# Kernel optimization log

Measured on AMD Instinct MI355X. Metric: run time of the kernel, lower is better.

The kernel has to match this reference:

```python
import jax, jax.numpy as jnp
import numpy as np
import math

H = 5120        # hidden_size
NH = 32         # num heads
HD = H // NH    # head_dim = 160
B = 1
S = 2048
TRAIN_SEQLEN = 8192
BASE = 10000.0


def _rotary_cos_sin(seq_len):
    # Eval-mode RotaryEmbedding: seq_len clamped to training_seqlen, NTK alpha + mscale (logN) scaling.
    eff = max(seq_len, TRAIN_SEQLEN)
    scale = eff / TRAIN_SEQLEN
    mscale = 1.0 if scale <= 1.0 else 0.1 * math.log(scale) + 1.0
    ntk_alpha = max(2 ** math.ceil(math.log(eff / 4096, 2) + 1) - 1, 1)
    base = BASE * ntk_alpha ** (HD / (HD - 2))
    inv_freq = 1.0 / base ** (np.arange(0, HD, 2, dtype=np.float64) / HD)
    t = np.arange(eff, dtype=np.float64)
    freqs = np.outer(t, inv_freq)              # [eff, HD/2]
    emb = np.concatenate([freqs, freqs], axis=-1)  # [eff, HD]
    cos = (mscale * np.cos(emb))[:seq_len].astype(np.float32)
    sin = (mscale * np.sin(emb))[:seq_len].astype(np.float32)
    return jnp.asarray(cos), jnp.asarray(sin)


def _rotate_half(x):
    x1, x2 = x[..., : HD // 2], x[..., HD // 2 :]
    return jnp.concatenate([-x2, x1], axis=-1)


def setup_inputs() -> dict:
    key = jax.random.key(0)
    ks = jax.random.split(key, 6)
    hidden_states = jax.random.normal(ks[0], (B, S, H), jnp.float32)
    residual = jax.random.normal(ks[1], (B, S, H), jnp.float32)
    # boolean causal mask, True = masked (matches masked_fill semantics)
    attention_mask = jnp.triu(jnp.ones((S, S), dtype=bool), k=1)[None, None]
    Wq = jax.random.normal(ks[2], (H, H), jnp.float32) * 0.02      # query: Linear(h, h, bias=False)
    Wkv = jax.random.normal(ks[3], (2 * H, H), jnp.float32) * 0.02  # key_value: Linear(h, 2h, bias=False)
    Wd = jax.random.normal(ks[4], (H, H), jnp.float32) * 0.02       # dense: Linear(h, h) with bias
    bd = jnp.zeros((H,), jnp.float32)
    return {
        "hidden_states": hidden_states,
        "residual": residual,
        "attention_mask": attention_mask,
        "Wq": Wq,
        "Wkv": Wkv,
        "Wd": Wd,
        "bd": bd,
    }


def reference(hidden_states, residual, attention_mask, Wq, Wkv, Wd, bd):
    b, s, h = hidden_states.shape
    # QKV projections (torch Linear: y = x @ W.T)
    q = jnp.einsum('bsh,oh->bso', hidden_states, Wq).reshape(b, s, NH, HD)
    kv = jnp.einsum('bsh,oh->bso', hidden_states, Wkv).reshape(b, s, NH, 2 * HD)
    k, v = kv[..., :HD], kv[..., HD:]
    # rotary embedding with logN mscale folded into cos/sin
    cos, sin = _rotary_cos_sin(s)               # [s, HD]
    cos = cos[None, :, None, :]
    sin = sin[None, :, None, :]
    q = q * cos + _rotate_half(q) * sin
    k = k * cos + _rotate_half(k) * sin
    inv_norm = 1.0 / math.sqrt(HD)
    scores = jnp.einsum('bqnd,bknd->bnqk', q, k) * inv_norm   # [b, nh, s, s]
    scores = jnp.where(attention_mask, jnp.finfo(scores.dtype).min, scores)
    probs = jax.nn.softmax(scores, axis=-1)
    # attention_dropout p=0.0 -> identity
    ctx = jnp.einsum('bnqk,bknd->bqnd', probs, v).reshape(b, s, h)
    out = ctx @ Wd.T + bd
    # dropout_add with hidden_dropout=0.0 (eval) -> residual + out
    return residual + out
```

## Files before the change

### kernel.cpp

```cpp
#include <hip/hip_runtime.h>
#include <cmath>

typedef unsigned short u16;
typedef unsigned int   u32;

using bf16x8 = __attribute__((ext_vector_type(8))) short;
using f32x4  = __attribute__((ext_vector_type(4))) float;

#define S_LEN 2048
#define NHEAD 32
#define HDIM  160
#define HID   5120
#define NQKV  15360

__device__ __forceinline__ f32x4 mfma16(bf16x8 a, bf16x8 b, f32x4 c) {
  return __builtin_amdgcn_mfma_f32_16x16x32_bf16(a, b, c, 0, 0, 0);
}

__device__ __forceinline__ u16 f2bf(float f) {
  u32 u = __builtin_bit_cast(u32, f);
  u += 0x7FFFu + ((u >> 16) & 1u);
  return (u16)(u >> 16);
}
__device__ __forceinline__ float bf2f(u16 h) {
  u32 u = ((u32)h) << 16;
  return __builtin_bit_cast(float, u);
}

__device__ __forceinline__ void gload16(const void* g, void* l) {
  __builtin_amdgcn_global_load_lds((const __attribute__((address_space(1))) void*)g,
                                   (__attribute__((address_space(3))) void*)l, 16, 0, 0);
}

__global__ void cvt_all_kernel(const float* __restrict__ hs, const float* __restrict__ Wq,
                               const float* __restrict__ Wkv, const float* __restrict__ Wd,
                               u16* __restrict__ Xb, u16* __restrict__ Wqkvb,
                               u16* __restrict__ Wdb) {
  const int n_hs = S_LEN * HID / 8;
  const int n_q  = HID * HID / 8;
  const int n_kv = 2 * HID * HID / 8;
  const int n_d  = HID * HID / 8;
  const int total = n_hs + n_q + n_kv + n_d;
  for (int i = blockIdx.x * 256 + threadIdx.x; i < total; i += gridDim.x * 256) {
    const float* src; u16* dst; int j = i;
    if (j < n_hs)                { src = hs;  dst = Xb; }
    else if ((j -= n_hs) < n_q)  { src = Wq;  dst = Wqkvb; }
    else if ((j -= n_q) < n_kv)  { src = Wkv; dst = Wqkvb + (size_t)HID * HID; }
    else { j -= n_kv;              src = Wd;  dst = Wdb; }
    float4 a = ((const float4*)src)[(size_t)j * 2];
    float4 b = ((const float4*)src)[(size_t)j * 2 + 1];
    uint4 o;
    o.x = (u32)f2bf(a.x) | ((u32)f2bf(a.y) << 16);
    o.y = (u32)f2bf(a.z) | ((u32)f2bf(a.w) << 16);
    o.z = (u32)f2bf(b.x) | ((u32)f2bf(b.y) << 16);
    o.w = (u32)f2bf(b.z) | ((u32)f2bf(b.w) << 16);
    ((uint4*)dst)[j] = o;
  }
}

__global__ void rope_table_kernel(float2* __restrict__ tab) {
  __shared__ double invf_s[80];
  int tid = threadIdx.x;
  if (tid < 80) {
    double base = 10000.0 * pow(3.0, 160.0 / 158.0);
    invf_s[tid] = pow(base, -((double)(2 * tid)) / 160.0);
  }
  __syncthreads();
  for (int i = blockIdx.x * 256 + tid; i < S_LEN * 80; i += gridDim.x * 256) {
    int s = i / 80, j = i % 80;
    double ang = fmod((double)s * invf_s[j], 6.283185307179586476925287);
    float a = (float)ang;
    tab[i] = make_float2(cosf(a), sinf(a));
  }
}

__global__ void rope_apply2_kernel(const u16* __restrict__ qkv, const float2* __restrict__ tab,
                                   u16* __restrict__ Qr, u16* __restrict__ Kr) {
  const int n = S_LEN * NHEAD * 80;
  int i = blockIdx.x * 256 + threadIdx.x;
  bool isK = i >= n;
  if (isK) i -= n;
  const u16* src = qkv + (isK ? HID : 0);
  int headStride = isK ? 2 * HDIM : HDIM;
  u16* dst = isK ? Kr : Qr;

  int dp = i % 80; int sh = i / 80; int h = sh % NHEAD; int s = sh / NHEAD;
  int d = 2 * dp;
  const u16* row = src + (size_t)s * NQKV + h * headStride;
  u32 q01 = *(const u32*)&row[d];
  u32 p01 = *(const u32*)&row[d < 80 ? d + 80 : d - 80];
  int j = (d < 80) ? d : d - 80;
  float2 cs0 = tab[s * 80 + j];
  float2 cs1 = tab[s * 80 + j + 1];
  float q0 = bf2f((u16)(q01 & 0xffff)), q1 = bf2f((u16)(q01 >> 16));
  float p0 = bf2f((u16)(p01 & 0xffff)), p1 = bf2f((u16)(p01 >> 16));
  float sgn = (d < 80) ? -1.f : 1.f;
  float o0 = q0 * cs0.x + sgn * p0 * cs0.y;
  float o1 = q1 * cs1.x + sgn * p1 * cs1.y;
  u32 o = (u32)f2bf(o0) | ((u32)f2bf(o1) << 16);
  *(u32*)&dst[((size_t)h * S_LEN + s) * HDIM + d] = o;
}

__global__ void vtrans_kernel(const u16* __restrict__ src, u16* __restrict__ Vt, int rowStride) {
  __shared__ u16 T[HDIM][72];
  int h = blockIdx.y; int s0 = blockIdx.x * 64; int tid = threadIdx.x;
  for (int i = tid; i < 64 * 80; i += 256) {
    int s = i / 80, dp = i % 80;
    u32 v = *(const u32*)&src[(size_t)(s0 + s) * rowStride + h * 320 + 2 * dp];
    T[2 * dp][s]     = (u16)(v & 0xffff);
    T[2 * dp + 1][s] = (u16)(v >> 16);
  }
  __syncthreads();
  for (int i = tid; i < HDIM * 32; i += 256) {
    int d = i / 32, sp = i % 32;
    u32 v = (u32)T[d][2 * sp] | ((u32)T[d][2 * sp + 1] << 16);
    *(u32*)&Vt[((size_t)h * HDIM + d) * S_LEN + s0 + 2 * sp] = v;
  }
}

template<int EPI>
__global__ __launch_bounds__(512, 4) void gemm256(
    const u16* __restrict__ A, const u16* __restrict__ Bm, void* __restrict__ Cout,
    int M, int N, int K, const float* __restrict__ bias, const float* __restrict__ resid)
{
  __shared__ u16 As[2][8192];
  __shared__ u16 Bs[2][4096];
  int tid = threadIdx.x;
  int w = tid >> 6, l = tid & 63, l15 = l & 15, l4 = l >> 4;
  int wr = w >> 1, wc = w & 1;

  int nbx = gridDim.x;
  int nwg = nbx * gridDim.y;
  int lin = blockIdx.y * nbx + blockIdx.x;
  int cpx = nwg >> 3;
  int swz = (lin & 7) * cpx + (lin >> 3);
  int bm = (swz / nbx) * 256, bn = (swz % nbx) * 128;

  int srow = tid >> 2;
  int scol = ((tid & 3) * 8) ^ ((srow & 8) ? 16 : 0);
  const u16* gA0 = A + (size_t)(bm + srow) * K + scol;
  const u16* gA1 = gA0 + (size_t)128 * K;
  const u16* gB  = Bm + (size_t)(bn + srow) * K + scol;
  int w512 = w * 512;

  f32x4 acc[4][4];
#pragma unroll
  for (int i = 0; i < 4; i++)
#pragma unroll
    for (int j = 0; j < 4; j++) acc[i][j] = f32x4{0.f, 0.f, 0.f, 0.f};

  int cA = (l4 * 8) ^ ((l15 & 8) ? 16 : 0);
  const int NT = K >> 5;
  int arow = wr * 64;
  int brow = wc * 64;

  auto STAGE = [&](int kt) { int p = kt & 1, ko = kt << 5;
    gload16(gA0 + ko, &As[p][w512]);
    gload16(gA1 + ko, &As[p][4096 + w512]);
    gload16(gB  + ko, &Bs[p][w512]);
  };

  STAGE(0);
  for (int kt = 0; kt < NT; ++kt) {
    int p = kt & 1;
    if (kt + 1 < NT) {
      STAGE(kt + 1);
      asm volatile("s_waitcnt vmcnt(3)" ::: "memory");
    } else {
      asm volatile("s_waitcnt vmcnt(0)" ::: "memory");
    }
    __builtin_amdgcn_s_barrier();

    bf16x8 aF[4], bF[4];
#pragma unroll
    for (int mi = 0; mi < 4; ++mi)
      aF[mi] = *(const bf16x8*)&As[p][(arow + mi * 16 + l15) * 32 + cA];
#pragma unroll
    for (int ni = 0; ni < 4; ++ni)
      bF[ni] = *(const bf16x8*)&Bs[p][(brow + ni * 16 + l15) * 32 + cA];
    __builtin_amdgcn_s_setprio(1);
#pragma unroll
    for (int mi = 0; mi < 4; ++mi)
#pragma unroll
      for (int ni = 0; ni < 4; ++ni)
        acc[mi][ni] = mfma16(aF[mi], bF[ni], acc[mi][ni]);
    __builtin_amdgcn_s_setprio(0);
    __builtin_amdgcn_s_barrier();
  }

#pragma unroll
  for (int mi = 0; mi < 4; ++mi)
#pragma unroll
    for (int ni = 0; ni < 4; ++ni) {
      int row0 = bm + wr * 64 + mi * 16 + l4 * 4;
      int col  = bn + wc * 64 + ni * 16 + l15;
      if (EPI == 0) {
        u16* C = (u16*)Cout;
#pragma unroll
        for (int r = 0; r < 4; r++) C[(size_t)(row0 + r) * N + col] = f2bf(acc[mi][ni][r]);
      } else {
        float* C = (float*)Cout;
        float b = bias[col];
#pragma unroll
        for (int r = 0; r < 4; r++) {
          size_t idx = (size_t)(row0 + r) * N + col;
          C[idx] = acc[mi][ni][r] + b + resid[idx];
        }
      }
    }
}

template<int EPI>
__global__ __launch_bounds__(256, 2) void gemm_bt(
    const u16* __restrict__ A, const u16* __restrict__ Bm, void* __restrict__ Cout,
    int M, int N, int K, const float* __restrict__ bias, const float* __restrict__ resid)
{
  int tid = threadIdx.x;
  int wv = tid >> 6, l = tid & 63, l15 = l & 15, l4 = l >> 4;
  int nbx = gridDim.x;
  int nwg = nbx * gridDim.y;
  int lin = blockIdx.y * nbx + blockIdx.x;
  int cpx = nwg >> 3;
  int swz = (lin & 7) * cpx + (lin >> 3);
  int bm = (swz / nbx) * 128, bn = (swz % nbx) * 128;

  __shared__ u16 As[128 * 32], Bs[128 * 32];
  f32x4 acc[4][4];
#pragma unroll
  for (int i = 0; i < 4; i++)
#pragma unroll
    for (int j = 0; j < 4; j++) acc[i][j] = f32x4{0.f, 0.f, 0.f, 0.f};

  int wm = (wv >> 1) * 64, wn = (wv & 1) * 64;
  const u16* gA = A + (size_t)(bm + (tid >> 2)) * K + (tid & 3) * 8;
  const u16* gB = Bm + (size_t)(bn + (tid >> 2)) * K + (tid & 3) * 8;
  u16* ldsA = As + wv * 16 * 32;
  u16* ldsB = Bs + wv * 16 * 32;

  for (int k0 = 0; k0 < K; k0 += 32) {
    __syncthreads();
    gload16(gA + k0, ldsA);
    gload16(gA + (size_t)64 * K + k0, ldsA + 64 * 32);
    gload16(gB + k0, ldsB);
    gload16(gB + (size_t)64 * K + k0, ldsB + 64 * 32);
    __syncthreads();
    bf16x8 af[4], bfr[4];
#pragma unroll
    for (int i = 0; i < 4; i++) af[i] = *(const bf16x8*)&As[(wm + i * 16 + l15) * 32 + l4 * 8];
#pragma unroll
    for (int i = 0; i < 4; i++) bfr[i] = *(const bf16x8*)&Bs[(wn + i * 16 + l15) * 32 + l4 * 8];
#pragma unroll
    for (int mi = 0; mi < 4; mi++)
#pragma unroll
      for (int ni = 0; ni < 4; ni++) acc[mi][ni] = mfma16(af[mi], bfr[ni], acc[mi][ni]);
  }

#pragma unroll
  for (int mi = 0; mi < 4; mi++)
#pragma unroll
    for (int ni = 0; ni < 4; ni++) {
      int row0 = bm + wm + mi * 16 + l4 * 4;
      int col  = bn + wn + ni * 16 + l15;
      if (EPI == 0) {
        u16* C = (u16*)Cout;
#pragma unroll
        for (int r = 0; r < 4; r++) C[(size_t)(row0 + r) * N + col] = f2bf(acc[mi][ni][r]);
      } else {
        float* C = (float*)Cout;
        float b = bias[col];
#pragma unroll
        for (int r = 0; r < 4; r++) {
          size_t idx = (size_t)(row0 + r) * N + col;
          C[idx] = acc[mi][ni][r] + b + resid[idx];
        }
      }
    }
}

__global__ __launch_bounds__(256, 2) void attn_kernel(
    const u16* __restrict__ Qr, const u16* __restrict__ Kr,
    const u16* __restrict__ Vt, u16* __restrict__ ctx)
{
  int lin = blockIdx.x;
  int h  = lin & 31;
  int qx = (lin < 256) ? (15 - (lin >> 5)) : ((lin - 256) >> 5);
  int q0 = qx * 128;
  int tid = threadIdx.x;
  int w = tid >> 6, l = tid & 63, l15 = l & 15, l4 = l >> 4;
  int qb = q0 + w * 32;

  __shared__ u16 Ks[64][164];
  __shared__ u16 Plds[4][32][68];

  const u16* Qh = Qr + (size_t)h * S_LEN * HDIM;
  const u16* Kh = Kr + (size_t)h * S_LEN * HDIM;
  const u16* Vh = Vt + (size_t)h * HDIM * S_LEN;

  bf16x8 aQ[2][5];
#pragma unroll
  for (int mi = 0; mi < 2; mi++)
#pragma unroll
    for (int kc = 0; kc < 5; kc++)
      aQ[mi][kc] = *(const bf16x8*)&Qh[(size_t)(qb + mi * 16 + l15) * HDIM + kc * 32 + l4 * 8];

  f32x4 accO[2][10];
#pragma unroll
  for (int mi = 0; mi < 2; mi++)
#pragma unroll
    for (int dt = 0; dt < 10; dt++) accO[mi][dt] = f32x4{0.f, 0.f, 0.f, 0.f};
  float mrun[2][4], lrun[2][4];
#pragma unroll
  for (int mi = 0; mi < 2; mi++)
#pragma unroll
    for (int r = 0; r < 4; r++) { mrun[mi][r] = -1e30f; lrun[mi][r] = 0.f; }

  const float c2 = 0.07905694150420949f * 1.44269504088896f;
  int Tend = 2 * qx + 2;

  {
    uint4 rg[5];
#pragma unroll
    for (int i = 0; i < 5; i++) {
      int u = tid + 256 * i;
      int row = u / 20, c = u % 20;
      rg[i] = *(const uint4*)&Kh[(size_t)row * HDIM + c * 8];
    }
#pragma unroll
    for (int i = 0; i < 5; i++) {
      int u = tid + 256 * i;
      int row = u / 20, c = u % 20;
      *(uint4*)&Ks[row][c * 8] = rg[i];
    }
  }
  __syncthreads();

  for (int t = 0; t < Tend; ++t) {
    int k0 = t * 64;
    bool more = (t + 1 < Tend);
    uint4 rg[5];
    if (more) {
      int k1 = k0 + 64;
#pragma unroll
      for (int i = 0; i < 5; i++) {
        int u = tid + 256 * i;
        int row = u / 20, c = u % 20;
        rg[i] = *(const uint4*)&Kh[(size_t)(k1 + row) * HDIM + c * 8];
      }
    }

    if (k0 <= qb + 31) {
      f32x4 s_[2][4];
#pragma unroll
      for (int mi = 0; mi < 2; mi++)
#pragma unroll
        for (int nt = 0; nt < 4; nt++) s_[mi][nt] = f32x4{0.f, 0.f, 0.f, 0.f};

#pragma unroll
      for (int kc = 0; kc < 5; kc++) {
        bf16x8 bK[4];
#pragma unroll
        for (int nt = 0; nt < 4; nt++)
          bK[nt] = *(const bf16x8*)&Ks[nt * 16 + l15][kc * 32 + l4 * 8];
        __builtin_amdgcn_s_setprio(1);
#pragma unroll
        for (int mi = 0; mi < 2; mi++)
#pragma unroll
          for (int nt = 0; nt < 4; nt++)
            s_[mi][nt] = mfma16(aQ[mi][kc], bK[nt], s_[mi][nt]);
        __builtin_amdgcn_s_setprio(0);
      }

      if (k0 + 63 > qb) {
#pragma unroll
        for (int mi = 0; mi < 2; mi++)
#pragma unroll
          for (int nt = 0; nt < 4; nt++)
#pragma unroll
            for (int r = 0; r < 4; r++) {
              int kk = k0 + nt * 16 + l15;
              int qq = qb + mi * 16 + l4 * 4 + r;
              if (kk > qq) s_[mi][nt][r] = -1e30f;
            }
      }

#pragma unroll
      for (int mi = 0; mi < 2; mi++) {
        float sf[4];
#pragma unroll
        for (int r = 0; r < 4; r++) {
          float v = fmaxf(fmaxf(s_[mi][0][r], s_[mi][1][r]), fmaxf(s_[mi][2][r], s_[mi][3][r]));
#pragma unroll
          for (int m = 1; m <= 8; m <<= 1) v = fmaxf(v, __shfl_xor(v, m));
          float mnew = fmaxf(mrun[mi][r], v);
          sf[r] = exp2f((mrun[mi][r] - mnew) * c2);
          mrun[mi][r] = mnew;
        }
        float rsum[4] = {0.f, 0.f, 0.f, 0.f};
#pragma unroll
        for (int nt = 0; nt < 4; nt++)
#pragma unroll
          for (int r = 0; r < 4; r++) {
            float p = exp2f((s_[mi][nt][r] - mrun[mi][r]) * c2);
            s_[mi][nt][r] = p;
            rsum[r] += p;
          }
#pragma unroll
        for (int r = 0; r < 4; r++) {
          float v = rsum[r];
#pragma unroll
          for (int m = 1; m <= 8; m <<= 1) v += __shfl_xor(v, m);
          lrun[mi][r] = lrun[mi][r] * sf[r] + v;
        }
#pragma unroll
        for (int dt = 0; dt < 10; dt++)
#pragma unroll
          for (int r = 0; r < 4; r++) accO[mi][dt][r] *= sf[r];
#pragma unroll
        for (int nt = 0; nt < 4; nt++)
#pragma unroll
          for (int r = 0; r < 4; r++)
            Plds[w][mi * 16 + l4 * 4 + r][nt * 16 + l15] = f2bf(s_[mi][nt][r]);
      }

#pragma unroll
      for (int kc = 0; kc < 2; kc++) {
        bf16x8 aP[2];
#pragma unroll
        for (int mi = 0; mi < 2; mi++)
          aP[mi] = *(const bf16x8*)&Plds[w][mi * 16 + l15][kc * 32 + l4 * 8];
        bf16x8 bV[10];
#pragma unroll
        for (int dt = 0; dt < 10; dt++)
          bV[dt] = *(const bf16x8*)&Vh[(size_t)(dt * 16 + l15) * S_LEN + k0 + kc * 32 + l4 * 8];
        __builtin_amdgcn_s_setprio(1);
#pragma unroll
        for (int dt = 0; dt < 10; dt++) {
          accO[0][dt] = mfma16(aP[0], bV[dt], accO[0][dt]);
          accO[1][dt] = mfma16(aP[1], bV[dt], accO[1][dt]);
        }
        __builtin_amdgcn_s_setprio(0);
      }
    }

    __builtin_amdgcn_s_barrier();
    if (more) {
#pragma unroll
      for (int i = 0; i < 5; i++) {
        int u = tid + 256 * i;
        int row = u / 20, c = u % 20;
        *(uint4*)&Ks[row][c * 8] = rg[i];
      }
      asm volatile("s_waitcnt lgkmcnt(0)" ::: "memory");
    }
    __builtin_amdgcn_s_barrier();
  }

#pragma unroll
  for (int mi = 0; mi < 2; mi++) {
    float inv[4];
#pragma unroll
    for (int r = 0; r < 4; r++) inv[r] = 1.0f / lrun[mi][r];
#pragma unroll
    for (int dt = 0; dt < 10; dt++)
#pragma unroll
      for (int r = 0; r < 4; r++) {
        int q = qb + mi * 16 + l4 * 4 + r;
        ctx[(size_t)q * HID + h * HDIM + dt * 16 + l15] = f2bf(accO[mi][dt][r] * inv[r]);
      }
  }
}

extern "C" void kernel_launch(void* const* d_in, const int* in_sizes, int n_in,
                              void* d_out, int out_size, void* d_ws, size_t ws_size,
                              hipStream_t stream) {
  const float* hs    = (const float*)d_in[0];
  const float* resid = (const float*)d_in[1];
  const float* Wq  = (const float*)d_in[3];
  const float* Wkv = (const float*)d_in[4];
  const float* Wd  = (const float*)d_in[5];
  const float* bd  = (const float*)d_in[6];
  float* out = (float*)d_out;

  char* ws = (char*)d_ws;
  const size_t SH = (size_t)S_LEN * HID;
  u16* Xb     = (u16*)(ws);                        size_t off = SH * 2;
  u16* Wqkvb  = (u16*)(ws + off);                  off += (size_t)3 * HID * HID * 2;
  u16* Wdb    = (u16*)(ws + off);                  off += (size_t)HID * HID * 2;
  u16* QKVraw = (u16*)(ws + off);                  off += (size_t)S_LEN * NQKV * 2;
  u16* Qr     = (u16*)(ws + off);                  off += SH * 2;
  u16* Kr     = (u16*)(ws + off);                  off += SH * 2;
  u16* Vt     = (u16*)(ws + off);                  off += SH * 2;
  u16* ctx    = (u16*)(ws + off);                  off += SH * 2;
  float2* tab = (float2*)(ws + off);               off += (size_t)S_LEN * 80 * 8;

  cvt_all_kernel<<<2048, 256, 0, stream>>>(hs, Wq, Wkv, Wd, Xb, Wqkvb, Wdb);

  rope_table_kernel<<<64, 256, 0, stream>>>(tab);

  gemm256<0><<<dim3(NQKV / 128, S_LEN / 256), 512, 0, stream>>>(
      Xb, Wqkvb, QKVraw, S_LEN, NQKV, HID, nullptr, nullptr);

  rope_apply2_kernel<<<2 * S_LEN * NHEAD * 80 / 256, 256, 0, stream>>>(QKVraw, tab, Qr, Kr);
  vtrans_kernel<<<dim3(S_LEN / 64, NHEAD), 256, 0, stream>>>(QKVraw + HID + HDIM, Vt, NQKV);

  attn_kernel<<<512, 256, 0, stream>>>(Qr, Kr, Vt, ctx);

  gemm_bt<1><<<dim3(HID / 128, S_LEN / 128), 256, 0, stream>>>(
      ctx, Wdb, out, S_LEN, HID, HID, bd, resid);
}
```

Before: 885.6 us.

## Load K fragments directly from global memory per wave, dropping LDS staging

Removes the shared-memory K tile and its register-prefetch double buffer along with the two block barriers per iteration. Each wave now reads its K MFMA operands straight from global memory and runs only its own causal trip count. This drops block-wide synchronisation and lets waves with shorter causal ranges finish early. In exchange, K is read four times per block from global/L2 instead of once, and there is no longer any prefetch to hide global load latency before the QK MFMAs.

```diff
diff --git a/kernel.cpp b/kernel.cpp
--- a/kernel.cpp
+++ b/kernel.cpp
@@ -289,7 +289,6 @@
   int w = tid >> 6, l = tid & 63, l15 = l & 15, l4 = l >> 4;
   int qb = q0 + w * 32;
 
-  __shared__ u16 Ks[64][164];
   __shared__ u16 Plds[4][32][68];
 
   const u16* Qh = Qr + (size_t)h * S_LEN * HDIM;
@@ -315,144 +314,102 @@
     for (int r = 0; r < 4; r++) { mrun[mi][r] = -1e30f; lrun[mi][r] = 0.f; }
 
   const float c2 = 0.07905694150420949f * 1.44269504088896f;
-  int Tend = 2 * qx + 2;
-
-  {
-    uint4 rg[5];
-#pragma unroll
-    for (int i = 0; i < 5; i++) {
-      int u = tid + 256 * i;
-      int row = u / 20, c = u % 20;
-      rg[i] = *(const uint4*)&Kh[(size_t)row * HDIM + c * 8];
-    }
-#pragma unroll
-    for (int i = 0; i < 5; i++) {
-      int u = tid + 256 * i;
-      int row = u / 20, c = u % 20;
-      *(uint4*)&Ks[row][c * 8] = rg[i];
-    }
-  }
-  __syncthreads();
-
-  for (int t = 0; t < Tend; ++t) {
+  int TendW = (qb + 31) / 64 + 1;
+
+  for (int t = 0; t < TendW; ++t) {
     int k0 = t * 64;
-    bool more = (t + 1 < Tend);
-    uint4 rg[5];
-    if (more) {
-      int k1 = k0 + 64;
-#pragma unroll
-      for (int i = 0; i < 5; i++) {
-        int u = tid + 256 * i;
-        int row = u / 20, c = u % 20;
-        rg[i] = *(const uint4*)&Kh[(size_t)(k1 + row) * HDIM + c * 8];
-      }
-    }
-
-    if (k0 <= qb + 31) {
-      f32x4 s_[2][4];
+
+    f32x4 s_[2][4];
+#pragma unroll
+    for (int mi = 0; mi < 2; mi++)
+#pragma unroll
+      for (int nt = 0; nt < 4; nt++) s_[mi][nt] = f32x4{0.f, 0.f, 0.f, 0.f};
+
+#pragma unroll
+    for (int kc = 0; kc < 5; kc++) {
+      bf16x8 bK[4];
+#pragma unroll
+      for (int nt = 0; nt < 4; nt++)
+        bK[nt] = *(const bf16x8*)&Kh[(size_t)(k0 + nt * 16 + l15) * HDIM + kc * 32 + l4 * 8];
+      __builtin_amdgcn_s_setprio(1);
 #pragma unroll
       for (int mi = 0; mi < 2; mi++)
 #pragma unroll
-        for (int nt = 0; nt < 4; nt++) s_[mi][nt] = f32x4{0.f, 0.f, 0.f, 0.f};
-
-#pragma unroll
-      for (int kc = 0; kc < 5; kc++) {
-        bf16x8 bK[4];
-#pragma unroll
         for (int nt = 0; nt < 4; nt++)
-          bK[nt] = *(const bf16x8*)&Ks[nt * 16 + l15][kc * 32 + l4 * 8];
-        __builtin_amdgcn_s_setprio(1);
-#pragma unroll
-        for (int mi = 0; mi < 2; mi++)
-#pragma unroll
-          for (int nt = 0; nt < 4; nt++)
-            s_[mi][nt] = mfma16(aQ[mi][kc], bK[nt], s_[mi][nt]);
-        __builtin_amdgcn_s_setprio(0);
-      }
-
-      if (k0 + 63 > qb) {
-#pragma unroll
-        for (int mi = 0; mi < 2; mi++)
-#pragma unroll
-          for (int nt = 0; nt < 4; nt++)
-#pragma unroll
-            for (int r = 0; r < 4; r++) {
-              int kk = k0 + nt * 16 + l15;
-              int qq = qb + mi * 16 + l4 * 4 + r;
-              if (kk > qq) s_[mi][nt][r] = -1e30f;
-            }
-      }
-
-#pragma unroll
-      for (int mi = 0; mi < 2; mi++) {
-        float sf[4];
+          s_[mi][nt] = mfma16(aQ[mi][kc], bK[nt], s_[mi][nt]);
+      __builtin_amdgcn_s_setprio(0);
+    }
+
+    if (k0 + 63 > qb) {
+#pragma unroll
+      for (int mi = 0; mi < 2; mi++)
+#pragma unroll
+        for (int nt = 0; nt < 4; nt++)
+#pragma unroll
+          for (int r = 0; r < 4; r++) {
+            int kk = k0 + nt * 16 + l15;
+            int qq = qb + mi * 16 + l4 * 4 + r;
+            if (kk > qq) s_[mi][nt][r] = -1e30f;
+          }
+    }
+
+#pragma unroll
+    for (int mi = 0; mi < 2; mi++) {
+      float sf[4];
+#pragma unroll
+      for (int r = 0; r < 4; r++) {
+        float v = fmaxf(fmaxf(s_[mi][0][r], s_[mi][1][r]), fmaxf(s_[mi][2][r], s_[mi][3][r]));
+#pragma unroll
+        for (int m = 1; m <= 8; m <<= 1) v = fmaxf(v, __shfl_xor(v, m));
+        float mnew = fmaxf(mrun[mi][r], v);
+        sf[r] = exp2f((mrun[mi][r] - mnew) * c2);
+        mrun[mi][r] = mnew;
+      }
+      float rsum[4] = {0.f, 0.f, 0.f, 0.f};
+#pragma unroll
+      for (int nt = 0; nt < 4; nt++)
 #pragma unroll
         for (int r = 0; r < 4; r++) {
-          float v = fmaxf(fmaxf(s_[mi][0][r], s_[mi][1][r]), fmaxf(s_[mi][2][r], s_[mi][3][r]));
-#pragma unroll
-          for (int m = 1; m <= 8; m <<= 1) v = fmaxf(v, __shfl_xor(v, m));
-          float mnew = fmaxf(mrun[mi][r], v);
-          sf[r] = exp2f((mrun[mi][r] - mnew) * c2);
-          mrun[mi][r] = mnew;
+          float p = exp2f((s_[mi][nt][r] - mrun[mi][r]) * c2);
+          s_[mi][nt][r] = p;
+          rsum[r] += p;
         }
-        float rsum[4] = {0.f, 0.f, 0.f, 0.f};
-#pragma unroll
-        for (int nt = 0; nt < 4; nt++)
-#pragma unroll
-          for (int r = 0; r < 4; r++) {
-            float p = exp2f((s_[mi][nt][r] - mrun[mi][r]) * c2);
-            s_[mi][nt][r] = p;
-            rsum[r] += p;
-          }
-#pragma unroll
-        for (int r = 0; r < 4; r++) {
-          float v = rsum[r];
-#pragma unroll
-          for (int m = 1; m <= 8; m <<= 1) v += __shfl_xor(v, m);
-          lrun[mi][r] = lrun[mi][r] * sf[r] + v;
-        }
-#pragma unroll
-        for (int dt = 0; dt < 10; dt++)
-#pragma unroll
-          for (int r = 0; r < 4; r++) accO[mi][dt][r] *= sf[r];
-#pragma unroll
-        for (int nt = 0; nt < 4; nt++)
-#pragma unroll
-          for (int r = 0; r < 4; r++)
-            Plds[w][mi * 16 + l4 * 4 + r][nt * 16 + l15] = f2bf(s_[mi][nt][r]);
-      }
-
-#pragma unroll
-      for (int kc = 0; kc < 2; kc++) {
-        bf16x8 aP[2];
-#pragma unroll
-        for (int mi = 0; mi < 2; mi++)
-          aP[mi] = *(const bf16x8*)&Plds[w][mi * 16 + l15][kc * 32 + l4 * 8];
-        bf16x8 bV[10];
-#pragma unroll
-        for (int dt = 0; dt < 10; dt++)
-          bV[dt] = *(const bf16x8*)&Vh[(size_t)(dt * 16 + l15) * S_LEN + k0 + kc * 32 + l4 * 8];
-        __builtin_amdgcn_s_setprio(1);
-#pragma unroll
-        for (int dt = 0; dt < 10; dt++) {
-          accO[0][dt] = mfma16(aP[0], bV[dt], accO[0][dt]);
-          accO[1][dt] = mfma16(aP[1], bV[dt], accO[1][dt]);
-        }
-        __builtin_amdgcn_s_setprio(0);
-      }
-    }
-
-    __builtin_amdgcn_s_barrier();
-    if (more) {
-#pragma unroll
-      for (int i = 0; i < 5; i++) {
-        int u = tid + 256 * i;
-        int row = u / 20, c = u % 20;
-        *(uint4*)&Ks[row][c * 8] = rg[i];
-      }
-      asm volatile("s_waitcnt lgkmcnt(0)" ::: "memory");
-    }
-    __builtin_amdgcn_s_barrier();
+#pragma unroll
+      for (int r = 0; r < 4; r++) {
+        float v = rsum[r];
+#pragma unroll
+        for (int m = 1; m <= 8; m <<= 1) v += __shfl_xor(v, m);
+        lrun[mi][r] = lrun[mi][r] * sf[r] + v;
+      }
+#pragma unroll
+      for (int dt = 0; dt < 10; dt++)
+#pragma unroll
+        for (int r = 0; r < 4; r++) accO[mi][dt][r] *= sf[r];
+#pragma unroll
+      for (int nt = 0; nt < 4; nt++)
+#pragma unroll
+        for (int r = 0; r < 4; r++)
+          Plds[w][mi * 16 + l4 * 4 + r][nt * 16 + l15] = f2bf(s_[mi][nt][r]);
+    }
+
+#pragma unroll
+    for (int kc = 0; kc < 2; kc++) {
+      bf16x8 aP[2];
+#pragma unroll
+      for (int mi = 0; mi < 2; mi++)
+        aP[mi] = *(const bf16x8*)&Plds[w][mi * 16 + l15][kc * 32 + l4 * 8];
+      bf16x8 bV[10];
+#pragma unroll
+      for (int dt = 0; dt < 10; dt++)
+        bV[dt] = *(const bf16x8*)&Vh[(size_t)(dt * 16 + l15) * S_LEN + k0 + kc * 32 + l4 * 8];
+      __builtin_amdgcn_s_setprio(1);
+#pragma unroll
+      for (int dt = 0; dt < 10; dt++) {
+        accO[0][dt] = mfma16(aP[0], bV[dt], accO[0][dt]);
+        accO[1][dt] = mfma16(aP[1], bV[dt], accO[1][dt]);
+      }
+      __builtin_amdgcn_s_setprio(0);
+    }
   }
 
 #pragma unroll
```

Measured after the change: 870.7 us. Within noise of the previous version (-1.7%).
